# Kernel tuning notes

Measured on AMD Instinct MI355X. Metric: run time of the kernel, lower is better.

Reference implementation:

```python
import math
import jax, jax.numpy as jnp
import numpy as np

B, S, D, H, DFF = 2, 2048, 2048, 16, 8192
DH = D // H
EPS = 1e-5


def setup_inputs() -> dict:
    key = jax.random.key(0)
    ks = jax.random.split(key, 12)
    std = 0.02
    inp = {
        "x": jax.random.normal(ks[0], (B, S, D), dtype=jnp.float32),
        # causal mask: 1 = allowed, 0 = masked
        "attn_mask": jnp.tril(jnp.ones((S, S), dtype=jnp.int32))[None, None],
        "ln1_g": jnp.ones((D,), jnp.float32),
        "ln1_b": jnp.zeros((D,), jnp.float32),
        "wq": jax.random.normal(ks[1], (D, D), jnp.float32) * std,
        "bq": jnp.zeros((D,), jnp.float32),
        "wk": jax.random.normal(ks[2], (D, D), jnp.float32) * std,
        "bk": jnp.zeros((D,), jnp.float32),
        "wv": jax.random.normal(ks[3], (D, D), jnp.float32) * std,
        "bv": jnp.zeros((D,), jnp.float32),
        "wo": jax.random.normal(ks[4], (D, D), jnp.float32) * std,
        "bo": jnp.zeros((D,), jnp.float32),
        "ln2_g": jnp.ones((D,), jnp.float32),
        "ln2_b": jnp.zeros((D,), jnp.float32),
        "w_in": jax.random.normal(ks[5], (D, DFF), jnp.float32) * std,
        "b_in": jnp.zeros((DFF,), jnp.float32),
        "w_out": jax.random.normal(ks[6], (DFF, D), jnp.float32) * std,
        "b_out": jnp.zeros((D,), jnp.float32),
    }
    return inp


def _layernorm(x, g, b):
    m = jnp.mean(x, axis=-1, keepdims=True)
    v = jnp.mean(jnp.square(x - m), axis=-1, keepdims=True)
    return (x - m) * jax.lax.rsqrt(v + EPS) * g + b


def _block(x, attn_mask, ln1_g, ln1_b, wq, bq, wk, bk, wv, bv, wo, bo,
           ln2_g, ln2_b, w_in, b_in, w_out, b_out):
    b_, s_, d_ = x.shape
    # --- attention sublayer (pre-norm) ---
    xn = _layernorm(x, ln1_g, ln1_b)
    q = (xn @ wq + bq).reshape(b_, s_, H, DH)
    k = (xn @ wk + bk).reshape(b_, s_, H, DH)
    v = (xn @ wv + bv).reshape(b_, s_, H, DH)
    scores = jnp.einsum("bqhd,bkhd->bhqk", q, k) / math.sqrt(DH)  # [B,H,S,S]
    scores = jnp.where(attn_mask == 0, -jnp.inf, scores)
    probs = jax.nn.softmax(scores, axis=-1)
    attn = jnp.einsum("bhqk,bkhd->bqhd", probs, v).reshape(b_, s_, d_)
    x = x + (attn @ wo + bo)
    # --- MLP sublayer (pre-norm) ---
    xn = _layernorm(x, ln2_g, ln2_b)
    h = jax.nn.gelu(xn @ w_in + b_in, approximate=False)
    x = x + (h @ w_out + b_out)
    return x


def reference(x, attn_mask, ln1_g, ln1_b, wq, bq, wk, bk, wv, bv, wo, bo,
              ln2_g, ln2_b, w_in, b_in, w_out, b_out):
    return _block(x, attn_mask, ln1_g, ln1_b, wq, bq, wk, bk, wv, bv, wo, bo,
                  ln2_g, ln2_b, w_in, b_in, w_out, b_out)
```

## Files before the change

### kernel.cpp

```cpp
#include <hip/hip_runtime.h>
#include <hip/hip_bf16.h>

#define BB   2
#define SS   2048
#define DD   2048
#define HH   16
#define DHH  128
#define DFF  8192
#define MM   (BB*SS)
#define QKD  6144

typedef __hip_bfloat16 bf16;
typedef __bf16 bf16x8 __attribute__((ext_vector_type(8)));
typedef float  f32x4 __attribute__((ext_vector_type(4)));

__device__ __forceinline__ void gl2lds16(const void* g, void* lds_uniform_base) {
    __builtin_amdgcn_global_load_lds(
        (const __attribute__((address_space(1))) void*)g,
        (__attribute__((address_space(3))) void*)lds_uniform_base,
        16, 0, 0);
}

__global__ __launch_bounds__(256) void ln_kernel(const float* __restrict__ x,
                                                 const float* __restrict__ g,
                                                 const float* __restrict__ b,
                                                 bf16* __restrict__ out) {
    int row = blockIdx.x, tid = threadIdx.x;
    const float4* xr = (const float4*)(x + (size_t)row * DD);
    float4 v0 = xr[tid];
    float4 v1 = xr[tid + 256];
    float s  = v0.x + v0.y + v0.z + v0.w + v1.x + v1.y + v1.z + v1.w;
    float s2 = v0.x*v0.x + v0.y*v0.y + v0.z*v0.z + v0.w*v0.w
             + v1.x*v1.x + v1.y*v1.y + v1.z*v1.z + v1.w*v1.w;
    #pragma unroll
    for (int m = 32; m >= 1; m >>= 1) { s += __shfl_xor(s, m); s2 += __shfl_xor(s2, m); }
    __shared__ float red[8];
    int wv = tid >> 6;
    if ((tid & 63) == 0) { red[wv] = s; red[wv + 4] = s2; }
    __syncthreads();
    s  = red[0] + red[1] + red[2] + red[3];
    s2 = red[4] + red[5] + red[6] + red[7];
    float mean = s * (1.0f / DD);
    float rs = rsqrtf(s2 * (1.0f / DD) - mean * mean + 1e-5f);
    bf16* o = out + (size_t)row * DD;
    int c0 = tid * 4, c1 = (tid + 256) * 4;
    float a0[4] = {v0.x, v0.y, v0.z, v0.w};
    float a1[4] = {v1.x, v1.y, v1.z, v1.w};
    #pragma unroll
    for (int j = 0; j < 4; j++) {
        o[c0 + j] = __float2bfloat16((a0[j] - mean) * rs * g[c0 + j] + b[c0 + j]);
        o[c1 + j] = __float2bfloat16((a1[j] - mean) * rs * g[c1 + j] + b[c1 + j]);
    }
}

__global__ __launch_bounds__(256) void transpose_cast(const float* __restrict__ W,
                                                      bf16* __restrict__ Wt,
                                                      int K, int N) {
    __shared__ float t[32][33];
    int n0 = blockIdx.x * 32, k0 = blockIdx.y * 32;
    int tx = threadIdx.x, ty = threadIdx.y;
    #pragma unroll
    for (int i = 0; i < 4; i++)
        t[ty + i * 8][tx] = W[(size_t)(k0 + ty + i * 8) * N + n0 + tx];
    __syncthreads();
    #pragma unroll
    for (int i = 0; i < 4; i++)
        Wt[(size_t)(n0 + ty + i * 8) * K + k0 + tx] = __float2bfloat16(t[tx][ty + i * 8]);
}

__global__ __launch_bounds__(256) void concat3(const float* __restrict__ a,
                                               const float* __restrict__ b,
                                               const float* __restrict__ c,
                                               float* __restrict__ o) {
    int i = blockIdx.x * 256 + threadIdx.x;
    o[i] = i < 2048 ? a[i] : (i < 4096 ? b[i - 2048] : c[i - 4096]);
}

__global__ __launch_bounds__(256) void transpose_v(const bf16* __restrict__ qkv,
                                                   bf16* __restrict__ vt) {
    __shared__ bf16 t[32][33];
    int s0 = blockIdx.x * 32, d0 = blockIdx.y * 32;
    int bh = blockIdx.z;
    int b = bh >> 4, h = bh & 15;
    int tx = threadIdx.x, ty = threadIdx.y;
    #pragma unroll
    for (int i = 0; i < 4; i++)
        t[ty + i * 8][tx] = qkv[(size_t)(b * SS + s0 + ty + i * 8) * QKD + 4096 + h * DHH + d0 + tx];
    __syncthreads();
    #pragma unroll
    for (int i = 0; i < 4; i++)
        vt[(size_t)((b * HH + h) * DHH + d0 + ty + i * 8) * SS + s0 + tx] = t[tx][ty + i * 8];
}

__global__ __launch_bounds__(256) void gemm_bt(const bf16* __restrict__ A,
                                               const bf16* __restrict__ Bt,
                                               const float* __restrict__ bias,
                                               const float* __restrict__ resid,
                                               void* __restrict__ Cout,
                                               int M, int N, int K, int epi) {
    __shared__ __align__(16) bf16 As[128 * 32];
    __shared__ __align__(16) bf16 Bs[128 * 32];
    __shared__ __align__(16) float Es[4 * 16 * 68];
    int tid = threadIdx.x;
    int lane = tid & 63, wave = tid >> 6;
    int quad = lane >> 4, l15 = lane & 15;
    int wm = wave >> 1, wn = wave & 1;
    int bm0 = blockIdx.y * 128, bn0 = blockIdx.x * 128;
    const bf16* Ag = A + (size_t)bm0 * K;
    const bf16* Bg = Bt + (size_t)bn0 * K;
    f32x4 acc[4][4] = {};

    for (int kt = 0; kt < K; kt += 32) {
        __syncthreads();
        #pragma unroll
        for (int i = 0; i < 2; i++) {
            int chunk = i * 256 + tid;
            int row = chunk >> 2, c8 = chunk & 3;
            gl2lds16(Ag + (size_t)row * K + kt + c8 * 8, As + (i * 256 + wave * 64) * 8);
        }
        #pragma unroll
        for (int i = 0; i < 2; i++) {
            int chunk = i * 256 + tid;
            int row = chunk >> 2, c8 = chunk & 3;
            gl2lds16(Bg + (size_t)row * K + kt + c8 * 8, Bs + (i * 256 + wave * 64) * 8);
        }
        __syncthreads();
        bf16x8 af[4], bfr[4];
        #pragma unroll
        for (int mt = 0; mt < 4; mt++)
            af[mt] = *(const bf16x8*)(const void*)&As[(wm * 64 + mt * 16 + l15) * 32 + quad * 8];
        #pragma unroll
        for (int nt = 0; nt < 4; nt++)
            bfr[nt] = *(const bf16x8*)(const void*)&Bs[(wn * 64 + nt * 16 + l15) * 32 + quad * 8];
        #pragma unroll
        for (int mt = 0; mt < 4; mt++)
            #pragma unroll
            for (int nt = 0; nt < 4; nt++)
                acc[mt][nt] = __builtin_amdgcn_mfma_f32_16x16x32_bf16(af[mt], bfr[nt], acc[mt][nt], 0, 0, 0);
    }

    if (epi == 1) {
        #pragma unroll
        for (int nt = 0; nt < 4; nt++) {
            int col = bn0 + wn * 64 + nt * 16 + l15;
            float bv = bias[col];
            #pragma unroll
            for (int mt = 0; mt < 4; mt++)
                #pragma unroll
                for (int r = 0; r < 4; r++) {
                    int row = bm0 + wm * 64 + mt * 16 + quad * 4 + r;
                    size_t idx = (size_t)row * N + col;
                    ((float*)Cout)[idx] = acc[mt][nt][r] + bv + resid[idx];
                }
        }
    } else {
        float bv[4];
        #pragma unroll
        for (int nt = 0; nt < 4; nt++) bv[nt] = bias[bn0 + wn * 64 + nt * 16 + l15];
        int rr = lane >> 2, cc = lane & 3;
        #pragma unroll
        for (int mt = 0; mt < 4; mt++) {
            #pragma unroll
            for (int nt = 0; nt < 4; nt++)
                #pragma unroll
                for (int r = 0; r < 4; r++)
                    Es[wave * 1088 + (quad * 4 + r) * 68 + nt * 16 + l15] = acc[mt][nt][r] + bv[nt];
            asm volatile("s_waitcnt lgkmcnt(0)" ::: "memory");
            float vals[16];
            #pragma unroll
            for (int j4 = 0; j4 < 4; j4++) {
                float4 f = *(const float4*)&Es[wave * 1088 + rr * 68 + cc * 16 + j4 * 4];
                vals[j4 * 4 + 0] = f.x; vals[j4 * 4 + 1] = f.y;
                vals[j4 * 4 + 2] = f.z; vals[j4 * 4 + 3] = f.w;
            }
            asm volatile("s_waitcnt lgkmcnt(0)" ::: "memory");
            union { bf16 h[16]; uint4 u[2]; } ob;
            #pragma unroll
            for (int j = 0; j < 16; j++) {
                float v = vals[j];
                if (epi == 2) v = 0.5f * v * (1.0f + erff(v * 0.70710678118654752f));
                ob.h[j] = __float2bfloat16(v);
            }
            int grow = bm0 + wm * 64 + mt * 16 + rr;
            int gcol = bn0 + wn * 64 + cc * 16;
            uint4* dst = (uint4*)((bf16*)Cout + (size_t)grow * N + gcol);
            dst[0] = ob.u[0];
            dst[1] = ob.u[1];
        }
    }
}

__global__ __launch_bounds__(512) void flash_attn(const bf16* __restrict__ qkv,
                                                  const bf16* __restrict__ vt,
                                                  bf16* __restrict__ out) {
    __shared__ __align__(16) bf16 Qs[128 * 128];
    __shared__ __align__(16) bf16 Ks[128 * 128];
    __shared__ __align__(16) bf16 Vs[128 * 128];
    __shared__ __align__(16) bf16 Ps[8 * 16 * 128];
    int tid = threadIdx.x;
    int lane = tid & 63, wave = tid >> 6;
    int quad = lane >> 4, l15 = lane & 15;
    int xr = blockIdx.x;
    int t = (xr & 1) ? (15 - (xr >> 1)) : (xr >> 1);
    int q0 = t * 128;
    int h = blockIdx.y, b = blockIdx.z;
    int jlast = t;
    const float scale = 0.088388347648318447f;

    int srow = tid >> 4;
    int sgrp = (tid & 15) ^ (srow & 15);

    const bf16* qb = qkv + h * DHH;
    const bf16* kb = qkv + 2048 + h * DHH;

    #pragma unroll
    for (int i = 0; i < 4; i++) {
        int row = i * 32 + srow;
        gl2lds16(qb + (size_t)(b * SS + q0 + row) * QKD + sgrp * 8,
                 Qs + i * 4096 + wave * 512);
    }

    f32x4 oacc[8] = {};
    float mrun[4] = {-1e30f, -1e30f, -1e30f, -1e30f};
    float lrun[4] = {0.f, 0.f, 0.f, 0.f};

    for (int j = 0; j <= jlast; j++) {
        __syncthreads();
        #pragma unroll
        for (int i = 0; i < 4; i++) {
            int row = i * 32 + srow;
            gl2lds16(kb + (size_t)(b * SS + j * 128 + row) * QKD + sgrp * 8,
                     Ks + i * 4096 + wave * 512);
        }
        #pragma unroll
        for (int i = 0; i < 4; i++) {
            int row = i * 32 + srow;
            gl2lds16(vt + (size_t)((b * HH + h) * DHH + row) * SS + j * 128 + sgrp * 8,
                     Vs + i * 4096 + wave * 512);
        }
        __syncthreads();

        f32x4 sacc[8] = {};
        bf16x8 aq[4];
        #pragma unroll
        for (int kc = 0; kc < 4; kc++)
            aq[kc] = *(const bf16x8*)(const void*)&Qs[(wave * 16 + l15) * 128 + (((kc * 4 + quad) ^ l15) * 8)];
        #pragma unroll
        for (int n = 0; n < 8; n++)
            #pragma unroll
            for (int kc = 0; kc < 4; kc++) {
                bf16x8 bk = *(const bf16x8*)(const void*)&Ks[(n * 16 + l15) * 128 + (((kc * 4 + quad) ^ l15) * 8)];
                sacc[n] = __builtin_amdgcn_mfma_f32_16x16x32_bf16(aq[kc], bk, sacc[n], 0, 0, 0);
            }

        float mx[4] = {-1e30f, -1e30f, -1e30f, -1e30f};
        #pragma unroll
        for (int n = 0; n < 8; n++)
            #pragma unroll
            for (int r = 0; r < 4; r++) {
                float v = sacc[n][r] * scale;
                if (j == jlast) {
                    int kl = n * 16 + l15;
                    int ql = wave * 16 + quad * 4 + r;
                    if (kl > ql) v = -1e30f;
                }
                sacc[n][r] = v;
                mx[r] = fmaxf(mx[r], v);
            }
        #pragma unroll
        for (int r = 0; r < 4; r++) {
            mx[r] = fmaxf(mx[r], __shfl_xor(mx[r], 1));
            mx[r] = fmaxf(mx[r], __shfl_xor(mx[r], 2));
            mx[r] = fmaxf(mx[r], __shfl_xor(mx[r], 4));
            mx[r] = fmaxf(mx[r], __shfl_xor(mx[r], 8));
        }
        float alpha[4], rsum[4];
        #pragma unroll
        for (int r = 0; r < 4; r++) {
            float mn = fmaxf(mrun[r], mx[r]);
            alpha[r] = __expf(mrun[r] - mn);
            mrun[r] = mn;
            rsum[r] = 0.f;
        }
        #pragma unroll
        for (int n = 0; n < 8; n++)
            #pragma unroll
            for (int r = 0; r < 4; r++) {
                float p = __expf(sacc[n][r] - mrun[r]);
                sacc[n][r] = p;
                rsum[r] += p;
            }
        #pragma unroll
        for (int r = 0; r < 4; r++) {
            rsum[r] += __shfl_xor(rsum[r], 1);
            rsum[r] += __shfl_xor(rsum[r], 2);
            rsum[r] += __shfl_xor(rsum[r], 4);
            rsum[r] += __shfl_xor(rsum[r], 8);
            lrun[r] = lrun[r] * alpha[r] + rsum[r];
        }
        #pragma unroll
        for (int n = 0; n < 8; n++)
            #pragma unroll
            for (int r = 0; r < 4; r++)
                oacc[n][r] *= alpha[r];

        #pragma unroll
        for (int n = 0; n < 8; n++)
            #pragma unroll
            for (int r = 0; r < 4; r++) {
                int rowp = quad * 4 + r;
                int g = 2 * n + (l15 >> 3);
                Ps[wave * 2048 + rowp * 128 + ((g ^ rowp) * 8) + (l15 & 7)] =
                    __float2bfloat16(sacc[n][r]);
            }
        asm volatile("s_waitcnt lgkmcnt(0)" ::: "memory");

        bf16x8 ap[4];
        #pragma unroll
        for (int kc = 0; kc < 4; kc++)
            ap[kc] = *(const bf16x8*)(const void*)&Ps[wave * 2048 + l15 * 128 + (((kc * 4 + quad) ^ l15) * 8)];
        #pragma unroll
        for (int n = 0; n < 8; n++)
            #pragma unroll
            for (int kc = 0; kc < 4; kc++) {
                bf16x8 bv = *(const bf16x8*)(const void*)&Vs[(n * 16 + l15) * 128 + (((kc * 4 + quad) ^ l15) * 8)];
                oacc[n] = __builtin_amdgcn_mfma_f32_16x16x32_bf16(ap[kc], bv, oacc[n], 0, 0, 0);
            }
    }

    #pragma unroll
    for (int n = 0; n < 8; n++)
        #pragma unroll
        for (int r = 0; r < 4; r++) {
            float v = oacc[n][r] / lrun[r];
            out[(size_t)(b * SS + q0 + wave * 16 + quad * 4 + r) * DD + h * DHH + n * 16 + l15] =
                __float2bfloat16(v);
        }
}

extern "C" void kernel_launch(void* const* d_in, const int* in_sizes, int n_in,
                              void* d_out, int out_size, void* d_ws, size_t ws_size,
                              hipStream_t stream) {
    (void)in_sizes; (void)n_in; (void)out_size; (void)ws_size;
    const float* x     = (const float*)d_in[0];
    const float* ln1_g = (const float*)d_in[2];
    const float* ln1_b = (const float*)d_in[3];
    const float* wq    = (const float*)d_in[4];
    const float* bq    = (const float*)d_in[5];
    const float* wk    = (const float*)d_in[6];
    const float* bk    = (const float*)d_in[7];
    const float* wv    = (const float*)d_in[8];
    const float* bv    = (const float*)d_in[9];
    const float* wo    = (const float*)d_in[10];
    const float* bo    = (const float*)d_in[11];
    const float* ln2_g = (const float*)d_in[12];
    const float* ln2_b = (const float*)d_in[13];
    const float* w_in  = (const float*)d_in[14];
    const float* b_in  = (const float*)d_in[15];
    const float* w_out = (const float*)d_in[16];
    const float* b_out = (const float*)d_in[17];
    float* out = (float*)d_out;

    char* ws = (char*)d_ws;
    const size_t MB = 1024 * 1024;
    bf16*  wt   = (bf16*)(ws + 0 * MB);
    bf16*  xn   = (bf16*)(ws + 32 * MB);
    bf16*  qkvb = (bf16*)(ws + 48 * MB);
    bf16*  vtb  = (bf16*)(ws + 96 * MB);
    float* x1   = (float*)(ws + 112 * MB);
    float* bcat = (float*)(ws + 144 * MB);
    bf16*  hb   = (bf16*)(ws + 48 * MB);
    bf16*  att  = xn;
    bf16*  xn2  = xn;

    dim3 t256(256), t32x8(32, 8);

    ln_kernel<<<MM, t256, 0, stream>>>(x, ln1_g, ln1_b, xn);

    transpose_cast<<<dim3(DD / 32, DD / 32), t32x8, 0, stream>>>(wq, wt, DD, DD);
    transpose_cast<<<dim3(DD / 32, DD / 32), t32x8, 0, stream>>>(wk, wt + 2048 * 2048, DD, DD);
    transpose_cast<<<dim3(DD / 32, DD / 32), t32x8, 0, stream>>>(wv, wt + 2 * 2048 * 2048, DD, DD);
    concat3<<<QKD / 256, t256, 0, stream>>>(bq, bk, bv, bcat);
    gemm_bt<<<dim3(QKD / 128, MM / 128), t256, 0, stream>>>(xn, wt, bcat, nullptr, qkvb, MM, QKD, DD, 0);

    transpose_v<<<dim3(SS / 32, DHH / 32, BB * HH), t32x8, 0, stream>>>(qkvb, vtb);

    flash_attn<<<dim3(SS / 128, HH, BB), dim3(512), 0, stream>>>(qkvb, vtb, att);

    transpose_cast<<<dim3(DD / 32, DD / 32), t32x8, 0, stream>>>(wo, wt, DD, DD);
    gemm_bt<<<dim3(DD / 128, MM / 128), t256, 0, stream>>>(att, wt, bo, x, x1, MM, DD, DD, 1);

    ln_kernel<<<MM, t256, 0, stream>>>(x1, ln2_g, ln2_b, xn2);

    transpose_cast<<<dim3(DFF / 32, DD / 32), t32x8, 0, stream>>>(w_in, wt, DD, DFF);
    gemm_bt<<<dim3(DFF / 128, MM / 128), t256, 0, stream>>>(xn2, wt, b_in, nullptr, hb, MM, DFF, DD, 2);

    transpose_cast<<<dim3(DD / 32, DFF / 32), t32x8, 0, stream>>>(w_out, wt, DFF, DD);
    gemm_bt<<<dim3(DD / 128, MM / 128), t256, 0, stream>>>(hb, wt, b_out, x1, out, MM, DD, DFF, 1);
}
```

Baseline: 1.079 ms.

## Replace GEMM with 512-thread multi-stage pipelined kernel using larger tiles and swizzled LDS

Replaces the single-buffered 128x128 GEMM with a templated 512-thread kernel that uses 256-wide N tiles (BM 256 or 128), a 4-slot LDS ring with 3 tiles prefetched via direct global-to-LDS loads, XOR-swizzled LDS layout, and split MFMA phases with setprio and explicit barriers. It also remaps block indices for XCD-aware scheduling. The aim is to hide global-load latency, raise data reuse per tile and cut LDS bank conflicts across all four GEMMs. Larger LDS use and the manual vmcnt accounting add occupancy and correctness risk.

```diff
diff --git a/kernel.cpp b/kernel.cpp
--- a/kernel.cpp
+++ b/kernel.cpp
@@ -92,52 +92,126 @@
         vt[(size_t)((b * HH + h) * DHH + d0 + ty + i * 8) * SS + s0 + tx] = t[tx][ty + i * 8];
 }
 
-__global__ __launch_bounds__(256) void gemm_bt(const bf16* __restrict__ A,
-                                               const bf16* __restrict__ Bt,
-                                               const float* __restrict__ bias,
-                                               const float* __restrict__ resid,
-                                               void* __restrict__ Cout,
-                                               int M, int N, int K, int epi) {
-    __shared__ __align__(16) bf16 As[128 * 32];
-    __shared__ __align__(16) bf16 Bs[128 * 32];
-    __shared__ __align__(16) float Es[4 * 16 * 68];
+template<int BM>
+__global__ __launch_bounds__(512, 2) void gemm_bt8(const bf16* __restrict__ A,
+                                                   const bf16* __restrict__ Bt,
+                                                   const float* __restrict__ bias,
+                                                   const float* __restrict__ resid,
+                                                   void* __restrict__ Cout,
+                                                   int M, int N, int K, int epi) {
+    constexpr int BN = 256;
+    constexpr int MT = BM / 32;
+    constexpr int MH = MT / 2;
+    constexpr int ASLOT = BM * 32;
+    constexpr int BSLOT = BN * 32;
+    __shared__ __align__(16) bf16 smem[4 * (ASLOT + BSLOT)];
+    bf16* As = smem;
+    bf16* Bs = smem + 4 * ASLOT;
+    float* Es = (float*)smem;
+
     int tid = threadIdx.x;
     int lane = tid & 63, wave = tid >> 6;
     int quad = lane >> 4, l15 = lane & 15;
-    int wm = wave >> 1, wn = wave & 1;
-    int bm0 = blockIdx.y * 128, bn0 = blockIdx.x * 128;
+    int wm = wave >> 2, wn = wave & 3;
+
+    int nbx = N / BN;
+    int lin = (int)blockIdx.x;
+    int cpx = (int)gridDim.x >> 3;
+    lin = (lin & 7) * cpx + (lin >> 3);
+    int bx = lin % nbx, by = lin / nbx;
+    int bm0 = by * BM, bn0 = bx * BN;
+
     const bf16* Ag = A + (size_t)bm0 * K;
     const bf16* Bg = Bt + (size_t)bn0 * K;
-    f32x4 acc[4][4] = {};
-
-    for (int kt = 0; kt < K; kt += 32) {
-        __syncthreads();
-        #pragma unroll
-        for (int i = 0; i < 2; i++) {
-            int chunk = i * 256 + tid;
-            int row = chunk >> 2, c8 = chunk & 3;
-            gl2lds16(Ag + (size_t)row * K + kt + c8 * 8, As + (i * 256 + wave * 64) * 8);
-        }
-        #pragma unroll
-        for (int i = 0; i < 2; i++) {
-            int chunk = i * 256 + tid;
-            int row = chunk >> 2, c8 = chunk & 3;
-            gl2lds16(Bg + (size_t)row * K + kt + c8 * 8, Bs + (i * 256 + wave * 64) * 8);
-        }
-        __syncthreads();
-        bf16x8 af[4], bfr[4];
-        #pragma unroll
-        for (int mt = 0; mt < 4; mt++)
-            af[mt] = *(const bf16x8*)(const void*)&As[(wm * 64 + mt * 16 + l15) * 32 + quad * 8];
-        #pragma unroll
-        for (int nt = 0; nt < 4; nt++)
-            bfr[nt] = *(const bf16x8*)(const void*)&Bs[(wn * 64 + nt * 16 + l15) * 32 + quad * 8];
-        #pragma unroll
-        for (int mt = 0; mt < 4; mt++)
-            #pragma unroll
-            for (int nt = 0; nt < 4; nt++)
-                acc[mt][nt] = __builtin_amdgcn_mfma_f32_16x16x32_bf16(af[mt], bfr[nt], acc[mt][nt], 0, 0, 0);
-    }
+
+    int srow = tid >> 2;
+    int grp = (tid & 3) ^ ((srow >> 1) & 3);
+    const bf16* aSrc0 = Ag + (size_t)srow * K + grp * 8;
+    const bf16* aSrc1 = Ag + (size_t)(128 + srow) * K + grp * 8;
+    const bf16* bSrc0 = Bg + (size_t)srow * K + grp * 8;
+    const bf16* bSrc1 = Bg + (size_t)(128 + srow) * K + grp * 8;
+
+    int T = K / 32;
+
+    auto stA0 = [&](int t) { gl2lds16(aSrc0 + t * 32, As + (t & 3) * ASLOT + wave * 512); };
+    auto stA1 = [&](int t) { gl2lds16(aSrc1 + t * 32, As + (t & 3) * ASLOT + 4096 + wave * 512); };
+    auto stB0 = [&](int t) { gl2lds16(bSrc0 + t * 32, Bs + (t & 3) * BSLOT + wave * 512); };
+    auto stB1 = [&](int t) { gl2lds16(bSrc1 + t * 32, Bs + (t & 3) * BSLOT + 4096 + wave * 512); };
+
+    #pragma unroll
+    for (int u = 0; u < 3; u++) {
+        if constexpr (BM == 256) { stA0(u); stA1(u); stB0(u); stB1(u); }
+        else                     { stA0(u); stB0(u); stB1(u); }
+    }
+    if constexpr (BM == 256) asm volatile("s_waitcnt vmcnt(8)" ::: "memory");
+    else                     asm volatile("s_waitcnt vmcnt(6)" ::: "memory");
+    __builtin_amdgcn_s_barrier();
+    __builtin_amdgcn_sched_barrier(0);
+
+    f32x4 acc[MT][4] = {};
+    int goff = (quad ^ ((l15 >> 1) & 3)) * 8;
+    int aro = (wm * (BM / 2) + l15) * 32 + goff;
+    int bro = (wn * 64 + l15) * 32 + goff;
+
+    for (int t = 0; t < T; ++t) {
+        const bf16* AsS = As + (t & 3) * ASLOT;
+        const bf16* BsS = Bs + (t & 3) * BSLOT;
+        int u = t + 3;
+        bf16x8 af[MH], bfr[4];
+
+        #pragma unroll
+        for (int m = 0; m < MH; m++)
+            af[m] = *(const bf16x8*)(const void*)&AsS[aro + m * 512];
+        #pragma unroll
+        for (int n = 0; n < 4; n++)
+            bfr[n] = *(const bf16x8*)(const void*)&BsS[bro + n * 512];
+        if (u < T) {
+            if constexpr (BM == 256) { stA0(u); stA1(u); }
+            else                     { stA0(u); stB0(u); }
+        }
+        __builtin_amdgcn_s_barrier();
+        __builtin_amdgcn_sched_barrier(0);
+        __builtin_amdgcn_s_setprio(1);
+        #pragma unroll
+        for (int m = 0; m < MH; m++)
+            #pragma unroll
+            for (int n = 0; n < 4; n++)
+                acc[m][n] = __builtin_amdgcn_mfma_f32_16x16x32_bf16(af[m], bfr[n], acc[m][n], 0, 0, 0);
+        __builtin_amdgcn_s_setprio(0);
+        __builtin_amdgcn_s_barrier();
+        __builtin_amdgcn_sched_barrier(0);
+
+        #pragma unroll
+        for (int m = 0; m < MH; m++)
+            af[m] = *(const bf16x8*)(const void*)&AsS[aro + (MH + m) * 512];
+        if (u < T) {
+            if constexpr (BM == 256) { stB0(u); stB1(u); }
+            else                     { stB1(u); }
+        }
+        __builtin_amdgcn_s_barrier();
+        __builtin_amdgcn_sched_barrier(0);
+        __builtin_amdgcn_s_setprio(1);
+        #pragma unroll
+        for (int m = 0; m < MH; m++)
+            #pragma unroll
+            for (int n = 0; n < 4; n++)
+                acc[MH + m][n] = __builtin_amdgcn_mfma_f32_16x16x32_bf16(af[m], bfr[n], acc[MH + m][n], 0, 0, 0);
+        __builtin_amdgcn_s_setprio(0);
+
+        if (t < T - 3) {
+            if constexpr (BM == 256) asm volatile("s_waitcnt vmcnt(8)" ::: "memory");
+            else                     asm volatile("s_waitcnt vmcnt(6)" ::: "memory");
+        } else if (t == T - 3) {
+            if constexpr (BM == 256) asm volatile("s_waitcnt vmcnt(4)" ::: "memory");
+            else                     asm volatile("s_waitcnt vmcnt(3)" ::: "memory");
+        } else if (t == T - 2) {
+            asm volatile("s_waitcnt vmcnt(0)" ::: "memory");
+        }
+        __builtin_amdgcn_s_barrier();
+        __builtin_amdgcn_sched_barrier(0);
+    }
+
+    __syncthreads();
 
     if (epi == 1) {
         #pragma unroll
@@ -145,10 +219,10 @@
             int col = bn0 + wn * 64 + nt * 16 + l15;
             float bv = bias[col];
             #pragma unroll
-            for (int mt = 0; mt < 4; mt++)
+            for (int mt = 0; mt < MT; mt++)
                 #pragma unroll
                 for (int r = 0; r < 4; r++) {
-                    int row = bm0 + wm * 64 + mt * 16 + quad * 4 + r;
+                    int row = bm0 + wm * (BM / 2) + mt * 16 + quad * 4 + r;
                     size_t idx = (size_t)row * N + col;
                     ((float*)Cout)[idx] = acc[mt][nt][r] + bv + resid[idx];
                 }
@@ -159,13 +233,14 @@
         for (int nt = 0; nt < 4; nt++) bv[nt] = bias[bn0 + wn * 64 + nt * 16 + l15];
         int rr = lane >> 2, cc = lane & 3;
         #pragma unroll
-        for (int mt = 0; mt < 4; mt++) {
+        for (int mt = 0; mt < MT; mt++) {
             #pragma unroll
             for (int nt = 0; nt < 4; nt++)
                 #pragma unroll
                 for (int r = 0; r < 4; r++)
                     Es[wave * 1088 + (quad * 4 + r) * 68 + nt * 16 + l15] = acc[mt][nt][r] + bv[nt];
             asm volatile("s_waitcnt lgkmcnt(0)" ::: "memory");
+            __builtin_amdgcn_sched_barrier(0);
             float vals[16];
             #pragma unroll
             for (int j4 = 0; j4 < 4; j4++) {
@@ -174,18 +249,19 @@
                 vals[j4 * 4 + 2] = f.z; vals[j4 * 4 + 3] = f.w;
             }
             asm volatile("s_waitcnt lgkmcnt(0)" ::: "memory");
-            union { bf16 h[16]; uint4 u[2]; } ob;
+            __builtin_amdgcn_sched_barrier(0);
+            union { bf16 h[16]; uint4 u4[2]; } ob;
             #pragma unroll
             for (int j = 0; j < 16; j++) {
                 float v = vals[j];
                 if (epi == 2) v = 0.5f * v * (1.0f + erff(v * 0.70710678118654752f));
                 ob.h[j] = __float2bfloat16(v);
             }
-            int grow = bm0 + wm * 64 + mt * 16 + rr;
+            int grow = bm0 + wm * (BM / 2) + mt * 16 + rr;
             int gcol = bn0 + wn * 64 + cc * 16;
             uint4* dst = (uint4*)((bf16*)Cout + (size_t)grow * N + gcol);
-            dst[0] = ob.u[0];
-            dst[1] = ob.u[1];
+            dst[0] = ob.u4[0];
+            dst[1] = ob.u4[1];
         }
     }
 }
@@ -314,6 +390,7 @@
                     __float2bfloat16(sacc[n][r]);
             }
         asm volatile("s_waitcnt lgkmcnt(0)" ::: "memory");
+        __builtin_amdgcn_sched_barrier(0);
 
         bf16x8 ap[4];
         #pragma unroll
@@ -373,7 +450,7 @@
     bf16*  att  = xn;
     bf16*  xn2  = xn;
 
-    dim3 t256(256), t32x8(32, 8);
+    dim3 t256(256), t32x8(32, 8), t512(512);
 
     ln_kernel<<<MM, t256, 0, stream>>>(x, ln1_g, ln1_b, xn);
 
@@ -381,20 +458,20 @@
     transpose_cast<<<dim3(DD / 32, DD / 32), t32x8, 0, stream>>>(wk, wt + 2048 * 2048, DD, DD);
     transpose_cast<<<dim3(DD / 32, DD / 32), t32x8, 0, stream>>>(wv, wt + 2 * 2048 * 2048, DD, DD);
     concat3<<<QKD / 256, t256, 0, stream>>>(bq, bk, bv, bcat);
-    gemm_bt<<<dim3(QKD / 128, MM / 128), t256, 0, stream>>>(xn, wt, bcat, nullptr, qkvb, MM, QKD, DD, 0);
+    gemm_bt8<256><<<dim3(384), t512, 0, stream>>>(xn, wt, bcat, nullptr, qkvb, MM, QKD, DD, 0);
 
     transpose_v<<<dim3(SS / 32, DHH / 32, BB * HH), t32x8, 0, stream>>>(qkvb, vtb);
 
-    flash_attn<<<dim3(SS / 128, HH, BB), dim3(512), 0, stream>>>(qkvb, vtb, att);
+    flash_attn<<<dim3(SS / 128, HH, BB), t512, 0, stream>>>(qkvb, vtb, att);
 
     transpose_cast<<<dim3(DD / 32, DD / 32), t32x8, 0, stream>>>(wo, wt, DD, DD);
-    gemm_bt<<<dim3(DD / 128, MM / 128), t256, 0, stream>>>(att, wt, bo, x, x1, MM, DD, DD, 1);
+    gemm_bt8<128><<<dim3(256), t512, 0, stream>>>(att, wt, bo, x, x1, MM, DD, DD, 1);
 
     ln_kernel<<<MM, t256, 0, stream>>>(x1, ln2_g, ln2_b, xn2);
 
     transpose_cast<<<dim3(DFF / 32, DD / 32), t32x8, 0, stream>>>(w_in, wt, DD, DFF);
-    gemm_bt<<<dim3(DFF / 128, MM / 128), t256, 0, stream>>>(xn2, wt, b_in, nullptr, hb, MM, DFF, DD, 2);
+    gemm_bt8<256><<<dim3(512), t512, 0, stream>>>(xn2, wt, b_in, nullptr, hb, MM, DFF, DD, 2);
 
     transpose_cast<<<dim3(DD / 32, DFF / 32), t32x8, 0, stream>>>(w_out, wt, DFF, DD);
-    gemm_bt<<<dim3(DD / 128, MM / 128), t256, 0, stream>>>(hb, wt, b_out, x1, out, MM, DD, DFF, 1);
-}
+    gemm_bt8<128><<<dim3(256), t512, 0, stream>>>(hb, wt, b_out, x1, out, MM, DD, DFF, 1);
+}
```

Result: faster. 884.6 us (-18.1%).

## Pipeline GEMM with triple-buffered LDS, swizzled layout, and XCD-aware block remap

Applied to the files above, without the earlier changes.

Replaces the single-buffered GEMM with a templated kernel that prefetches two K-tiles ahead into a three-slot LDS ring. It uses explicit vmcnt waits and barriers so global loads overlap the MFMA work. The LDS tiles are XOR-swizzled to reduce bank conflicts, and the linear block index is remapped across eight groups to improve L2 locality per XCD. The QKV and MLP-in GEMMs now use 512-thread 128x256 tiles, and MFMA sections raise wave priority. This adds more LDS pressure and fragile hand-tuned wait counts.

```diff
diff --git a/kernel.cpp b/kernel.cpp
--- a/kernel.cpp
+++ b/kernel.cpp
@@ -92,52 +92,103 @@
         vt[(size_t)((b * HH + h) * DHH + d0 + ty + i * 8) * SS + s0 + tx] = t[tx][ty + i * 8];
 }
 
-__global__ __launch_bounds__(256) void gemm_bt(const bf16* __restrict__ A,
-                                               const bf16* __restrict__ Bt,
-                                               const float* __restrict__ bias,
-                                               const float* __restrict__ resid,
-                                               void* __restrict__ Cout,
-                                               int M, int N, int K, int epi) {
-    __shared__ __align__(16) bf16 As[128 * 32];
-    __shared__ __align__(16) bf16 Bs[128 * 32];
-    __shared__ __align__(16) float Es[4 * 16 * 68];
+template<int THREADS, int BM, int BN>
+__global__ __launch_bounds__(THREADS, (THREADS == 512 ? 4 : 3))
+void gemm_p(const bf16* __restrict__ A,
+            const bf16* __restrict__ Bt,
+            const float* __restrict__ bias,
+            const float* __restrict__ resid,
+            void* __restrict__ Cout,
+            int M, int N, int K, int epi) {
+    constexpr int NWN    = BN / 64;
+    constexpr int ASLOT  = BM * 32;
+    constexpr int BSLOT  = BN * 32;
+    constexpr int ALOADS = BM * 4 / THREADS;
+    constexpr int BLOADS = BN * 4 / THREADS;
+    constexpr int LPT    = ALOADS + BLOADS;
+    __shared__ __align__(16) bf16 smem[3 * (ASLOT + BSLOT)];
+    bf16* As = smem;
+    bf16* Bs = smem + 3 * ASLOT;
+    float* Es = (float*)smem;
+
     int tid = threadIdx.x;
     int lane = tid & 63, wave = tid >> 6;
     int quad = lane >> 4, l15 = lane & 15;
-    int wm = wave >> 1, wn = wave & 1;
-    int bm0 = blockIdx.y * 128, bn0 = blockIdx.x * 128;
+    int wm = wave / NWN, wn = wave % NWN;
+
+    int nbx = N / BN;
+    int lin = (int)blockIdx.x;
+    int cpx = (int)gridDim.x >> 3;
+    lin = (lin & 7) * cpx + (lin >> 3);
+    int bx = lin % nbx, by = lin / nbx;
+    int bm0 = by * BM, bn0 = bx * BN;
+
     const bf16* Ag = A + (size_t)bm0 * K;
     const bf16* Bg = Bt + (size_t)bn0 * K;
+
+    int srow = tid >> 2;
+    int grp = (tid & 3) ^ ((srow >> 1) & 3);
+
+    auto stage = [&](int u, int slot) {
+        #pragma unroll
+        for (int i = 0; i < ALOADS; i++)
+            gl2lds16(Ag + (size_t)(i * (THREADS / 4) + srow) * K + u * 32 + grp * 8,
+                     As + slot * ASLOT + i * THREADS * 8 + wave * 512);
+        #pragma unroll
+        for (int i = 0; i < BLOADS; i++)
+            gl2lds16(Bg + (size_t)(i * (THREADS / 4) + srow) * K + u * 32 + grp * 8,
+                     Bs + slot * BSLOT + i * THREADS * 8 + wave * 512);
+    };
+
+    int T = K / 32;
+
+    stage(0, 0);
+    stage(1, 1);
+    if constexpr (LPT == 3) asm volatile("s_waitcnt vmcnt(3)" ::: "memory");
+    else                    asm volatile("s_waitcnt vmcnt(4)" ::: "memory");
+    __builtin_amdgcn_s_barrier();
+    __builtin_amdgcn_sched_barrier(0);
+
     f32x4 acc[4][4] = {};
-
-    for (int kt = 0; kt < K; kt += 32) {
-        __syncthreads();
-        #pragma unroll
-        for (int i = 0; i < 2; i++) {
-            int chunk = i * 256 + tid;
-            int row = chunk >> 2, c8 = chunk & 3;
-            gl2lds16(Ag + (size_t)row * K + kt + c8 * 8, As + (i * 256 + wave * 64) * 8);
-        }
-        #pragma unroll
-        for (int i = 0; i < 2; i++) {
-            int chunk = i * 256 + tid;
-            int row = chunk >> 2, c8 = chunk & 3;
-            gl2lds16(Bg + (size_t)row * K + kt + c8 * 8, Bs + (i * 256 + wave * 64) * 8);
-        }
-        __syncthreads();
+    int goff = (quad ^ ((l15 >> 1) & 3)) * 8;
+    int aro = (wm * 64 + l15) * 32 + goff;
+    int bro = (wn * 64 + l15) * 32 + goff;
+
+    int sl = 0;
+    for (int t = 0; t < T; ++t) {
+        const bf16* AsS = As + sl * ASLOT;
+        const bf16* BsS = Bs + sl * BSLOT;
         bf16x8 af[4], bfr[4];
         #pragma unroll
-        for (int mt = 0; mt < 4; mt++)
-            af[mt] = *(const bf16x8*)(const void*)&As[(wm * 64 + mt * 16 + l15) * 32 + quad * 8];
-        #pragma unroll
-        for (int nt = 0; nt < 4; nt++)
-            bfr[nt] = *(const bf16x8*)(const void*)&Bs[(wn * 64 + nt * 16 + l15) * 32 + quad * 8];
-        #pragma unroll
-        for (int mt = 0; mt < 4; mt++)
-            #pragma unroll
-            for (int nt = 0; nt < 4; nt++)
-                acc[mt][nt] = __builtin_amdgcn_mfma_f32_16x16x32_bf16(af[mt], bfr[nt], acc[mt][nt], 0, 0, 0);
+        for (int m = 0; m < 4; m++)
+            af[m] = *(const bf16x8*)(const void*)&AsS[aro + m * 512];
+        #pragma unroll
+        for (int n = 0; n < 4; n++)
+            bfr[n] = *(const bf16x8*)(const void*)&BsS[bro + n * 512];
+        __builtin_amdgcn_s_barrier();
+        __builtin_amdgcn_sched_barrier(0);
+        __builtin_amdgcn_s_setprio(1);
+        #pragma unroll
+        for (int m = 0; m < 4; m++)
+            #pragma unroll
+            for (int n = 0; n < 4; n++)
+                acc[m][n] = __builtin_amdgcn_mfma_f32_16x16x32_bf16(af[m], bfr[n], acc[m][n], 0, 0, 0);
+        __builtin_amdgcn_s_setprio(0);
+        int u = t + 2;
+        int su = sl + 2; if (su >= 3) su -= 3;
+        if (u < T) stage(u, su);
+        if (t < T - 2) {
+            if constexpr (LPT == 3) asm volatile("s_waitcnt vmcnt(3)" ::: "memory");
+            else                    asm volatile("s_waitcnt vmcnt(4)" ::: "memory");
+        } else if (t == T - 2) {
+            asm volatile("s_waitcnt vmcnt(0)" ::: "memory");
+        }
+        __builtin_amdgcn_s_barrier();
+        __builtin_amdgcn_sched_barrier(0);
+        sl = (sl == 2) ? 0 : sl + 1;
     }
+
+    __syncthreads();
 
     if (epi == 1) {
         #pragma unroll
@@ -166,6 +217,7 @@
                 for (int r = 0; r < 4; r++)
                     Es[wave * 1088 + (quad * 4 + r) * 68 + nt * 16 + l15] = acc[mt][nt][r] + bv[nt];
             asm volatile("s_waitcnt lgkmcnt(0)" ::: "memory");
+            __builtin_amdgcn_sched_barrier(0);
             float vals[16];
             #pragma unroll
             for (int j4 = 0; j4 < 4; j4++) {
@@ -174,7 +226,8 @@
                 vals[j4 * 4 + 2] = f.z; vals[j4 * 4 + 3] = f.w;
             }
             asm volatile("s_waitcnt lgkmcnt(0)" ::: "memory");
-            union { bf16 h[16]; uint4 u[2]; } ob;
+            __builtin_amdgcn_sched_barrier(0);
+            union { bf16 h[16]; uint4 u4[2]; } ob;
             #pragma unroll
             for (int j = 0; j < 16; j++) {
                 float v = vals[j];
@@ -184,8 +237,8 @@
             int grow = bm0 + wm * 64 + mt * 16 + rr;
             int gcol = bn0 + wn * 64 + cc * 16;
             uint4* dst = (uint4*)((bf16*)Cout + (size_t)grow * N + gcol);
-            dst[0] = ob.u[0];
-            dst[1] = ob.u[1];
+            dst[0] = ob.u4[0];
+            dst[1] = ob.u4[1];
         }
     }
 }
@@ -314,6 +367,7 @@
                     __float2bfloat16(sacc[n][r]);
             }
         asm volatile("s_waitcnt lgkmcnt(0)" ::: "memory");
+        __builtin_amdgcn_sched_barrier(0);
 
         bf16x8 ap[4];
         #pragma unroll
@@ -373,7 +427,7 @@
     bf16*  att  = xn;
     bf16*  xn2  = xn;
 
-    dim3 t256(256), t32x8(32, 8);
+    dim3 t256(256), t32x8(32, 8), t512(512);
 
     ln_kernel<<<MM, t256, 0, stream>>>(x, ln1_g, ln1_b, xn);
 
@@ -381,20 +435,20 @@
     transpose_cast<<<dim3(DD / 32, DD / 32), t32x8, 0, stream>>>(wk, wt + 2048 * 2048, DD, DD);
     transpose_cast<<<dim3(DD / 32, DD / 32), t32x8, 0, stream>>>(wv, wt + 2 * 2048 * 2048, DD, DD);
     concat3<<<QKD / 256, t256, 0, stream>>>(bq, bk, bv, bcat);
-    gemm_bt<<<dim3(QKD / 128, MM / 128), t256, 0, stream>>>(xn, wt, bcat, nullptr, qkvb, MM, QKD, DD, 0);
+    gemm_p<512, 128, 256><<<dim3(768), t512, 0, stream>>>(xn, wt, bcat, nullptr, qkvb, MM, QKD, DD, 0);
 
     transpose_v<<<dim3(SS / 32, DHH / 32, BB * HH), t32x8, 0, stream>>>(qkvb, vtb);
 
-    flash_attn<<<dim3(SS / 128, HH, BB), dim3(512), 0, stream>>>(qkvb, vtb, att);
+    flash_attn<<<dim3(SS / 128, HH, BB), t512, 0, stream>>>(qkvb, vtb, att);
 
     transpose_cast<<<dim3(DD / 32, DD / 32), t32x8, 0, stream>>>(wo, wt, DD, DD);
-    gemm_bt<<<dim3(DD / 128, MM / 128), t256, 0, stream>>>(att, wt, bo, x, x1, MM, DD, DD, 1);
+    gemm_p<256, 128, 128><<<dim3(512), t256, 0, stream>>>(att, wt, bo, x, x1, MM, DD, DD, 1);
 
     ln_kernel<<<MM, t256, 0, stream>>>(x1, ln2_g, ln2_b, xn2);
 
     transpose_cast<<<dim3(DFF / 32, DD / 32), t32x8, 0, stream>>>(w_in, wt, DD, DFF);
-    gemm_bt<<<dim3(DFF / 128, MM / 128), t256, 0, stream>>>(xn2, wt, b_in, nullptr, hb, MM, DFF, DD, 2);
+    gemm_p<512, 128, 256><<<dim3(1024), t512, 0, stream>>>(xn2, wt, b_in, nullptr, hb, MM, DFF, DD, 2);
 
     transpose_cast<<<dim3(DD / 32, DFF / 32), t32x8, 0, stream>>>(w_out, wt, DFF, DD);
-    gemm_bt<<<dim3(DD / 128, MM / 128), t256, 0, stream>>>(hb, wt, b_out, x1, out, MM, DD, DFF, 1);
-}
+    gemm_p<256, 128, 128><<<dim3(512), t256, 0, stream>>>(hb, wt, b_out, x1, out, MM, DD, DFF, 1);
+}
```

Result: faster. 893.3 us (-17.2%).
